# Kernel tuning notes

Hardware: AMD Instinct MI355X
Metric: run time of the kernel (lower is better)

The kernel has to match this reference:

```python
import jax, jax.numpy as jnp
import numpy as np

EMBED = 1024
HEADS = 16
HEAD_DIM = EMBED // HEADS


def setup_inputs() -> dict:
    key = jax.random.key(0)
    ks = jax.random.split(key, 12)
    N, S, E = 4, 2048, EMBED
    scale = 1.0 / np.sqrt(E)
    inp = {
        "values": jax.random.normal(ks[0], (N, S, E), dtype=jnp.float32),
        "keys": jax.random.normal(ks[1], (N, S, E), dtype=jnp.float32),
        "query": jax.random.normal(ks[2], (N, S, E), dtype=jnp.float32),
        "mask": jnp.ones((N, 1, 1, S), dtype=jnp.int32),
        # Linear params: y = x @ W + b (W stored as [in, out])
        "Wv": jax.random.normal(ks[3], (E, E), dtype=jnp.float32) * scale,
        "bv": jnp.zeros((E,), dtype=jnp.float32),
        "Wk": jax.random.normal(ks[4], (E, E), dtype=jnp.float32) * scale,
        "bk": jnp.zeros((E,), dtype=jnp.float32),
        "Wq": jax.random.normal(ks[5], (E, E), dtype=jnp.float32) * scale,
        "bq": jnp.zeros((E,), dtype=jnp.float32),
        "Wo": jax.random.normal(ks[6], (E, E), dtype=jnp.float32) * scale,
        "bo": jnp.zeros((E,), dtype=jnp.float32),
    }
    return inp


def reference(values, keys, query, mask, Wv, bv, Wk, bk, Wq, bq, Wo, bo):
    N, Q, E = query.shape
    V = values.shape[1]
    K = keys.shape[1]
    v = (values @ Wv + bv).reshape(N, V, HEADS, HEAD_DIM)
    k = (keys @ Wk + bk).reshape(N, K, HEADS, HEAD_DIM)
    q = (query @ Wq + bq).reshape(N, Q, HEADS, HEAD_DIM)
    # energy: [N, H, Q, K]
    energy = jnp.einsum("nqhd,nkhd->nhqk", q, k)
    energy = jnp.where(mask == 0, jnp.float32(-1e20), energy)
    # NOTE: original scales by sqrt(embed_size), not sqrt(head_dim)
    attn = jax.nn.softmax(energy / jnp.sqrt(jnp.float32(E)), axis=3)
    out = jnp.einsum("nhql,nlhd->nqhd", attn, v).reshape(N, Q, E)
    return out @ Wo + bo
```

## Files before the change

kernel.cpp:

```cpp
#include <hip/hip_runtime.h>

#define H 16
#define DH 64
#define S 2048
#define E 1024
#define NB 4

typedef short short8_t __attribute__((ext_vector_type(8)));
typedef float float4_t __attribute__((ext_vector_type(4)));
typedef float float16_t __attribute__((ext_vector_type(16)));

__device__ inline unsigned short f2bf(float f) {
    union { float f; unsigned u; } v; v.f = f;
    unsigned r = v.u + 0x7fffu + ((v.u >> 16) & 1u);
    return (unsigned short)(r >> 16);
}

__device__ __forceinline__ unsigned pk_bf16(float a, float b) {
    union { float f; unsigned u; } ua, ub;
    ua.f = a; ub.f = b;
    unsigned ra = ua.u + 0x7fffu + ((ua.u >> 16) & 1u);
    unsigned rb = ub.u + 0x7fffu + ((ub.u >> 16) & 1u);
    return __builtin_amdgcn_perm(rb, ra, 0x07060302u);
}

__device__ __forceinline__ unsigned cvt_pk_bf16(float a, float b) {
    unsigned r;
    asm("v_cvt_pk_bf16_f32 %0, %1, %2" : "=v"(r) : "v"(a), "v"(b));
    return r;
}

__device__ __forceinline__ float16_t mfma32(short8_t a, short8_t b, float16_t c) {
    return __builtin_amdgcn_mfma_f32_32x32x16_bf16(a, b, c, 0, 0, 0);
}

__device__ __forceinline__ void async_copy16(const unsigned short* g, unsigned short* l) {
    __builtin_amdgcn_global_load_lds(
        (const __attribute__((address_space(1))) unsigned int*)g,
        (__attribute__((address_space(3))) unsigned int*)l, 16, 0, 0);
}

__global__ __launch_bounds__(256) void xcvt_kernel(
    const float* __restrict__ v, const float* __restrict__ k,
    const float* __restrict__ q, unsigned short* __restrict__ xv,
    unsigned short* __restrict__ xk, unsigned short* __restrict__ xq)
{
    const int z = blockIdx.y;
    const float* src = (z == 0) ? v : (z == 1) ? k : q;
    unsigned short* dst = (z == 0) ? xv : (z == 1) ? xk : xq;
    size_t i0 = ((size_t)blockIdx.x * 256 + threadIdx.x) * 8;
    float4 f0 = *reinterpret_cast<const float4*>(src + i0);
    float4 f1 = *reinterpret_cast<const float4*>(src + i0 + 4);
    uint4 o;
    o.x = pk_bf16(f0.x, f0.y); o.y = pk_bf16(f0.z, f0.w);
    o.z = pk_bf16(f1.x, f1.y); o.w = pk_bf16(f1.z, f1.w);
    *reinterpret_cast<uint4*>(dst + i0) = o;
}

__global__ __launch_bounds__(256) void wcvt_kernel(
    const float* __restrict__ Wv, const float* __restrict__ Wk,
    const float* __restrict__ Wq, const float* __restrict__ Wo,
    unsigned short* __restrict__ Wt)
{
    __shared__ float tile[64][65];
    const float* W = (blockIdx.z == 0) ? Wv : (blockIdx.z == 1) ? Wk
                   : (blockIdx.z == 2) ? Wq : Wo;
    unsigned short* out = Wt + (size_t)blockIdx.z * (E * E);
    const int k0 = blockIdx.x * 64, n0 = blockIdx.y * 64;
    const int tid = threadIdx.x;
#pragma unroll
    for (int i = 0; i < 4; ++i) {
        int c = i * 256 + tid;
        int kl = c >> 4, nl4 = (c & 15) * 4;
        float4 v = *reinterpret_cast<const float4*>(W + (size_t)(k0 + kl) * E + n0 + nl4);
        tile[kl][nl4 + 0] = v.x; tile[kl][nl4 + 1] = v.y;
        tile[kl][nl4 + 2] = v.z; tile[kl][nl4 + 3] = v.w;
    }
    __syncthreads();
#pragma unroll
    for (int i = 0; i < 4; ++i) {
        int c = i * 256 + tid;
        int nl = c >> 4, kl4 = (c & 15) * 4;
        ushort4 o;
        o.x = f2bf(tile[kl4 + 0][nl]); o.y = f2bf(tile[kl4 + 1][nl]);
        o.z = f2bf(tile[kl4 + 2][nl]); o.w = f2bf(tile[kl4 + 3][nl]);
        *reinterpret_cast<ushort4*>(out + (size_t)(n0 + nl) * E + k0 + kl4) = o;
    }
}

template<int MODE>
__global__ __launch_bounds__(256) void proj_kernel(
    const unsigned short* __restrict__ A, const unsigned short* __restrict__ WT,
    const float* __restrict__ bias, unsigned short* __restrict__ out)
{
    __shared__ __align__(16) unsigned short As[2][128][64];
    __shared__ __align__(16) unsigned short Bs[2][128][64];

    const int tid = threadIdx.x;
    const int wlin = blockIdx.y * 8 + blockIdx.x;
    const int wid = (wlin & 7) * 64 + (wlin >> 3);
    const int n0 = (wid & 7) * 128;
    const int m0 = (wid >> 3) * 128;
    const int wave = tid >> 6, lane = tid & 63;
    const int wm = wave >> 1, wn = wave & 1;
    const int quad = lane >> 4, l16 = lane & 15;
    const int r8 = lane >> 3;
    const int c8 = (lane & 7) ^ (r8 & 7);

    float4_t acc[4][4];
#pragma unroll
    for (int i = 0; i < 4; ++i)
#pragma unroll
        for (int j = 0; j < 4; ++j) { float4_t z = {0.f,0.f,0.f,0.f}; acc[i][j] = z; }

#pragma unroll
    for (int j = 0; j < 4; ++j) {
        int row = wave * 32 + j * 8 + r8;
        async_copy16(A  + (size_t)(m0 + row) * E + c8 * 8, &As[0][wave * 32 + j * 8][0]);
        async_copy16(WT + (size_t)(n0 + row) * E + c8 * 8, &Bs[0][wave * 32 + j * 8][0]);
    }

    for (int it = 0; it < 16; ++it) {
        const int cur = it & 1, nxt = cur ^ 1;
        __syncthreads();

        if (it < 15) {
            const int kn = (it + 1) * 64;
#pragma unroll
            for (int j = 0; j < 4; ++j) {
                int row = wave * 32 + j * 8 + r8;
                async_copy16(A  + (size_t)(m0 + row) * E + kn + c8 * 8, &As[nxt][wave * 32 + j * 8][0]);
                async_copy16(WT + (size_t)(n0 + row) * E + kn + c8 * 8, &Bs[nxt][wave * 32 + j * 8][0]);
            }
        }
#pragma unroll
        for (int kk = 0; kk < 2; ++kk) {
            short8_t a[4], b[4];
#pragma unroll
            for (int mi = 0; mi < 4; ++mi)
                a[mi] = *reinterpret_cast<const short8_t*>(
                    &As[cur][wm * 64 + mi * 16 + l16][((kk * 4 + quad) ^ (l16 & 7)) * 8]);
#pragma unroll
            for (int nj = 0; nj < 4; ++nj)
                b[nj] = *reinterpret_cast<const short8_t*>(
                    &Bs[cur][wn * 64 + nj * 16 + l16][((kk * 4 + quad) ^ (l16 & 7)) * 8]);
#pragma unroll
            for (int x = 0; x < 4; ++x)
#pragma unroll
                for (int y = 0; y < 4; ++y) {
                    if constexpr (MODE == 0)
                        acc[x][y] = __builtin_amdgcn_mfma_f32_16x16x32_bf16(b[x], a[y], acc[x][y], 0, 0, 0);
                    else
                        acc[x][y] = __builtin_amdgcn_mfma_f32_16x16x32_bf16(a[x], b[y], acc[x][y], 0, 0, 0);
                }
        }
    }

    if constexpr (MODE == 0) {
#pragma unroll
        for (int x = 0; x < 4; ++x) {
            float4 bb = *reinterpret_cast<const float4*>(&bias[n0 + wn * 64 + x * 16 + quad * 4]);
#pragma unroll
            for (int y = 0; y < 4; ++y) {
                int m = m0 + wm * 64 + y * 16 + l16;
                int nn = m >> 11, s = m & 2047;
                int sp = (s & ~12) | (((s >> 2) & 1) << 3) | (((s >> 3) & 1) << 2);
#pragma unroll
                for (int r = 0; r < 4; ++r) {
                    int gcol = n0 + wn * 64 + x * 16 + quad * 4 + r;
                    int h = gcol >> 6, d = gcol & 63;
                    float val = acc[x][y][r] + ((const float*)&bb)[r];
                    out[(((size_t)(nn * H + h)) * DH + d) * S + sp] = f2bf(val);
                }
            }
        }
    } else {
#pragma unroll
        for (int x = 0; x < 4; ++x) {
#pragma unroll
            for (int y = 0; y < 4; ++y) {
                int gcol = n0 + wn * 64 + y * 16 + l16;
                float bvv = bias[gcol];
                int h = gcol >> 6, d = gcol & 63;
#pragma unroll
                for (int r = 0; r < 4; ++r) {
                    int gm = m0 + wm * 64 + x * 16 + quad * 4 + r;
                    float val = acc[x][y][r] + bvv;
                    int nn = gm >> 11, s = gm & 2047;
                    out[(((size_t)(nn * H + h)) * S + s) * DH + d] = f2bf(val);
                }
            }
        }
    }
}

__global__ __launch_bounds__(256, 4) void flash_kernel(
    const unsigned short* __restrict__ Qb, const unsigned short* __restrict__ Kb,
    const unsigned short* __restrict__ VTb, const int* __restrict__ mask,
    unsigned short* __restrict__ AO)
{
    __shared__ __align__(16) unsigned short Ks[2][64][64];
    __shared__ __align__(16) unsigned short Vs[2][64][64];
    __shared__ __align__(16) float am[2][64];
    __shared__ __align__(16) float lbuf[4][32];

    const int tid = threadIdx.x;
    const int wave = tid >> 6, lane = tid & 63;
    const int l32 = lane & 31, hf = lane >> 5;
    const int r8 = lane >> 3;
    const int c8 = (lane & 7) ^ (r8 & 7);

    const int wlin = blockIdx.y * 16 + blockIdx.x;
    const int wid = (wlin & 7) * 128 + (wlin >> 3);
    const int qt = wid & 15;
    const int nh = wid >> 4;
    const int n = nh >> 4, h = nh & 15;
    const size_t hb = (size_t)nh * S * DH;
    const unsigned short* Qh = Qb + hb;
    const unsigned short* Kh = Kb + hb;
    const unsigned short* Vh = VTb + hb;
    const int* mp = mask + n * S;

    const float c1 = 0.03125f * 1.4426950408889634f;
    const float C2_UNMASK = -23.083120654223414f;
    const float C2_MASK   = -1.44e20f;

    short8_t qa[4];
#pragma unroll
    for (int ks = 0; ks < 4; ++ks) {
        int row = qt * 128 + wave * 32 + l32;
        qa[ks] = *reinterpret_cast<const short8_t*>(Qh + (size_t)row * DH + ks * 16 + hf * 8);
    }

    float16_t o[2];
#pragma unroll
    for (int nb = 0; nb < 2; ++nb)
#pragma unroll
        for (int i = 0; i < 16; ++i) o[nb][i] = 0.f;
    float lsum = 0.f;

#pragma unroll
    for (int j = 0; j < 2; ++j) {
        int row = wave * 16 + j * 8 + r8;
        async_copy16(Kh + (size_t)row * DH + c8 * 8, &Ks[0][wave * 16 + j * 8][0]);
        async_copy16(Vh + (size_t)row * S + c8 * 8,  &Vs[0][wave * 16 + j * 8][0]);
    }
    if (tid < 64) am[0][tid] = (mp[tid] == 0) ? C2_MASK : C2_UNMASK;

    for (int it = 0; it < 32; ++it) {
        const int cur = it & 1, nxt = cur ^ 1;
        __syncthreads();

        const int kn = (it < 31) ? (it + 1) * 64 : 0;
#pragma unroll
        for (int j = 0; j < 2; ++j) {
            int row = wave * 16 + j * 8 + r8;
            async_copy16(Kh + (size_t)(kn + row) * DH + c8 * 8, &Ks[nxt][wave * 16 + j * 8][0]);
            async_copy16(Vh + (size_t)row * S + kn + c8 * 8,    &Vs[nxt][wave * 16 + j * 8][0]);
        }
        if (tid < 64) am[nxt][tid] = (mp[kn + tid] == 0) ? C2_MASK : C2_UNMASK;

        unsigned w[2][4][2];
#pragma unroll
        for (int kvb = 0; kvb < 2; ++kvb) {
            float16_t st;
#pragma unroll
            for (int i = 0; i < 16; ++i) st[i] = 0.f;
            __builtin_amdgcn_s_setprio(1);
#pragma unroll
            for (int ks = 0; ks < 4; ++ks) {
                short8_t ak = *reinterpret_cast<const short8_t*>(
                    &Ks[cur][kvb * 32 + l32][((ks * 2 + hf) ^ (l32 & 7)) * 8]);
                st = mfma32(ak, qa[ks], st);
            }
            __builtin_amdgcn_s_setprio(0);
#pragma unroll
            for (int g = 0; g < 4; ++g) {
                float4 c2v = *reinterpret_cast<const float4*>(&am[cur][kvb * 32 + g * 8 + hf * 4]);
                float p0 = __builtin_amdgcn_exp2f(st[g * 4 + 0] * c1 + c2v.x);
                float p1 = __builtin_amdgcn_exp2f(st[g * 4 + 1] * c1 + c2v.y);
                float p2 = __builtin_amdgcn_exp2f(st[g * 4 + 2] * c1 + c2v.z);
                float p3 = __builtin_amdgcn_exp2f(st[g * 4 + 3] * c1 + c2v.w);
                lsum += (p0 + p1) + (p2 + p3);
                w[kvb][g][0] = cvt_pk_bf16(p0, p1);
                w[kvb][g][1] = cvt_pk_bf16(p2, p3);
            }
        }

        __builtin_amdgcn_s_setprio(1);
#pragma unroll
        for (int ks2 = 0; ks2 < 4; ++ks2) {
            const int kvb = ks2 >> 1, t = ks2 & 1;
            union { unsigned u[4]; short8_t s; } pu;
            pu.u[0] = w[kvb][t * 2][0];     pu.u[1] = w[kvb][t * 2][1];
            pu.u[2] = w[kvb][t * 2 + 1][0]; pu.u[3] = w[kvb][t * 2 + 1][1];
#pragma unroll
            for (int nb = 0; nb < 2; ++nb) {
                const int d = nb * 32 + l32;
                short8_t vb = *reinterpret_cast<const short8_t*>(
                    &Vs[cur][d][((kvb * 4 + t * 2 + hf) ^ (d & 7)) * 8]);
                o[nb] = mfma32(pu.s, vb, o[nb]);
            }
        }
        __builtin_amdgcn_s_setprio(0);
    }

    lsum += __shfl_xor(lsum, 32);
    if (lane < 32) lbuf[wave][lane] = lsum;

#pragma unroll
    for (int g = 0; g < 4; ++g) {
        float4 dn = *reinterpret_cast<const float4*>(&lbuf[wave][g * 8 + hf * 4]);
#pragma unroll
        for (int r = 0; r < 4; ++r) {
            float invl = __builtin_amdgcn_rcpf(((const float*)&dn)[r]);
            int row = g * 8 + hf * 4 + r;
            int qrow = qt * 128 + wave * 32 + row;
            size_t gm = (size_t)n * S + qrow;
#pragma unroll
            for (int nb = 0; nb < 2; ++nb) {
                int col = h * DH + nb * 32 + l32;
                AO[gm * E + col] = f2bf(o[nb][g * 4 + r] * invl);
            }
        }
    }
}

__global__ __launch_bounds__(256) void ogemm_kernel(
    const unsigned short* __restrict__ A, const unsigned short* __restrict__ WT,
    const float* __restrict__ bias, float* __restrict__ out)
{
    __shared__ __align__(16) unsigned short As[2][128][64];
    __shared__ __align__(16) unsigned short Bs[2][128][64];

    const int tid = threadIdx.x;
    const int wlin = blockIdx.y * 8 + blockIdx.x;
    const int wid = (wlin & 7) * 64 + (wlin >> 3);
    const int n0 = (wid & 7) * 128;
    const int m0 = (wid >> 3) * 128;
    const int wave = tid >> 6, lane = tid & 63;
    const int wm = wave >> 1, wn = wave & 1;
    const int quad = lane >> 4, l16 = lane & 15;
    const int r8 = lane >> 3;
    const int c8 = (lane & 7) ^ (r8 & 7);

    float4_t acc[4][4];
#pragma unroll
    for (int i = 0; i < 4; ++i)
#pragma unroll
        for (int j = 0; j < 4; ++j) { float4_t z = {0.f,0.f,0.f,0.f}; acc[i][j] = z; }

#pragma unroll
    for (int j = 0; j < 4; ++j) {
        int row = wave * 32 + j * 8 + r8;
        async_copy16(A  + (size_t)(m0 + row) * E + c8 * 8, &As[0][wave * 32 + j * 8][0]);
        async_copy16(WT + (size_t)(n0 + row) * E + c8 * 8, &Bs[0][wave * 32 + j * 8][0]);
    }

    for (int it = 0; it < 16; ++it) {
        const int cur = it & 1, nxt = cur ^ 1;
        __syncthreads();

        if (it < 15) {
            const int kn = (it + 1) * 64;
#pragma unroll
            for (int j = 0; j < 4; ++j) {
                int row = wave * 32 + j * 8 + r8;
                async_copy16(A  + (size_t)(m0 + row) * E + kn + c8 * 8, &As[nxt][wave * 32 + j * 8][0]);
                async_copy16(WT + (size_t)(n0 + row) * E + kn + c8 * 8, &Bs[nxt][wave * 32 + j * 8][0]);
            }
        }
#pragma unroll
        for (int kk = 0; kk < 2; ++kk) {
            short8_t a[4], b[4];
#pragma unroll
            for (int mi = 0; mi < 4; ++mi)
                a[mi] = *reinterpret_cast<const short8_t*>(
                    &As[cur][wm * 64 + mi * 16 + l16][((kk * 4 + quad) ^ (l16 & 7)) * 8]);
#pragma unroll
            for (int nj = 0; nj < 4; ++nj)
                b[nj] = *reinterpret_cast<const short8_t*>(
                    &Bs[cur][wn * 64 + nj * 16 + l16][((kk * 4 + quad) ^ (l16 & 7)) * 8]);
#pragma unroll
            for (int mi = 0; mi < 4; ++mi)
#pragma unroll
                for (int nj = 0; nj < 4; ++nj)
                    acc[mi][nj] = __builtin_amdgcn_mfma_f32_16x16x32_bf16(a[mi], b[nj], acc[mi][nj], 0, 0, 0);
        }
    }
#pragma unroll
    for (int mi = 0; mi < 4; ++mi)
#pragma unroll
        for (int nj = 0; nj < 4; ++nj) {
            int gcol = n0 + wn * 64 + nj * 16 + l16;
            float bvv = bias[gcol];
#pragma unroll
            for (int r = 0; r < 4; ++r) {
                int gm = m0 + wm * 64 + mi * 16 + quad * 4 + r;
                out[(size_t)gm * E + gcol] = acc[mi][nj][r] + bvv;
            }
        }
}

extern "C" void kernel_launch(void* const* d_in, const int* in_sizes, int n_in,
                              void* d_out, int out_size, void* d_ws, size_t ws_size,
                              hipStream_t stream) {
    const float* values = (const float*)d_in[0];
    const float* keys   = (const float*)d_in[1];
    const float* query  = (const float*)d_in[2];
    const int*   mask   = (const int*)d_in[3];
    const float* Wv = (const float*)d_in[4];  const float* bv = (const float*)d_in[5];
    const float* Wk = (const float*)d_in[6];  const float* bk = (const float*)d_in[7];
    const float* Wq = (const float*)d_in[8];  const float* bq = (const float*)d_in[9];
    const float* Wo = (const float*)d_in[10]; const float* bo = (const float*)d_in[11];
    float* out = (float*)d_out;

    char* ws = (char*)d_ws;
    unsigned short* Wt = (unsigned short*)ws;
    unsigned short* xv = (unsigned short*)(ws + 8388608);
    unsigned short* xk = (unsigned short*)(ws + 25165824);
    unsigned short* xq = (unsigned short*)(ws + 41943040);
    unsigned short* vt = (unsigned short*)(ws + 58720256);
    unsigned short* kb = xv;
    unsigned short* qb = xk;
    unsigned short* ao = xq;

    xcvt_kernel<<<dim3(4096, 3), 256, 0, stream>>>(values, keys, query, xv, xk, xq);
    wcvt_kernel<<<dim3(16, 16, 4), 256, 0, stream>>>(Wv, Wk, Wq, Wo, Wt);
    proj_kernel<0><<<dim3(8, 64), 256, 0, stream>>>(xv, Wt,           bv, vt);
    proj_kernel<1><<<dim3(8, 64), 256, 0, stream>>>(xk, Wt + 1048576, bk, kb);
    proj_kernel<1><<<dim3(8, 64), 256, 0, stream>>>(xq, Wt + 2097152, bq, qb);
    flash_kernel<<<dim3(16, 64), 256, 0, stream>>>(qb, kb, vt, mask, ao);
    ogemm_kernel<<<dim3(8, 64), 256, 0, stream>>>(ao, Wt + 3145728, bo, out);
}
```

Before: 343.5 us.

## Fuse fp32-to-bf16 input conversion into a single batched QKV projection kernel

Drops the separate activation conversion kernel. The projection GEMM now loads fp32 inputs straight into registers, converts them to bf16 and writes them to LDS, with the next tile's loads issued before the MFMA work. The three Q/K/V projection launches become one launch using blockIdx.z, and the workgroup swizzle is removed from both the projection and output GEMMs. This saves a full round trip of the bf16 activations through HBM plus two launches, at the cost of doubled global read bytes per A tile, more register pressure, and a runtime branch on z inside the MFMA loop.

```diff
diff --git a/kernel.cpp b/kernel.cpp
--- a/kernel.cpp
+++ b/kernel.cpp
@@ -38,23 +38,6 @@
     __builtin_amdgcn_global_load_lds(
         (const __attribute__((address_space(1))) unsigned int*)g,
         (__attribute__((address_space(3))) unsigned int*)l, 16, 0, 0);
-}
-
-__global__ __launch_bounds__(256) void xcvt_kernel(
-    const float* __restrict__ v, const float* __restrict__ k,
-    const float* __restrict__ q, unsigned short* __restrict__ xv,
-    unsigned short* __restrict__ xk, unsigned short* __restrict__ xq)
-{
-    const int z = blockIdx.y;
-    const float* src = (z == 0) ? v : (z == 1) ? k : q;
-    unsigned short* dst = (z == 0) ? xv : (z == 1) ? xk : xq;
-    size_t i0 = ((size_t)blockIdx.x * 256 + threadIdx.x) * 8;
-    float4 f0 = *reinterpret_cast<const float4*>(src + i0);
-    float4 f1 = *reinterpret_cast<const float4*>(src + i0 + 4);
-    uint4 o;
-    o.x = pk_bf16(f0.x, f0.y); o.y = pk_bf16(f0.z, f0.w);
-    o.z = pk_bf16(f1.x, f1.y); o.w = pk_bf16(f1.z, f1.w);
-    *reinterpret_cast<uint4*>(dst + i0) = o;
 }
 
 __global__ __launch_bounds__(256) void wcvt_kernel(
@@ -88,35 +71,59 @@
     }
 }
 
-template<int MODE>
-__global__ __launch_bounds__(256) void proj_kernel(
-    const unsigned short* __restrict__ A, const unsigned short* __restrict__ WT,
-    const float* __restrict__ bias, unsigned short* __restrict__ out)
+__global__ __launch_bounds__(256) void qkvproj_kernel(
+    const float* __restrict__ Va, const float* __restrict__ Ka,
+    const float* __restrict__ Qa, const unsigned short* __restrict__ Wt,
+    const float* __restrict__ bv, const float* __restrict__ bk,
+    const float* __restrict__ bq, unsigned short* __restrict__ vt,
+    unsigned short* __restrict__ kbo, unsigned short* __restrict__ qbo)
 {
     __shared__ __align__(16) unsigned short As[2][128][64];
     __shared__ __align__(16) unsigned short Bs[2][128][64];
 
+    const int z = blockIdx.z;
+    const float* Ag = (z == 0) ? Va : (z == 1) ? Ka : Qa;
+    const unsigned short* WT = Wt + (size_t)z * (E * E);
+    const float* bias = (z == 0) ? bv : (z == 1) ? bk : bq;
+    unsigned short* out = (z == 0) ? vt : (z == 1) ? kbo : qbo;
+
     const int tid = threadIdx.x;
-    const int wlin = blockIdx.y * 8 + blockIdx.x;
-    const int wid = (wlin & 7) * 64 + (wlin >> 3);
-    const int n0 = (wid & 7) * 128;
-    const int m0 = (wid >> 3) * 128;
+    const int m0 = blockIdx.y * 128;
+    const int n0 = blockIdx.x * 128;
     const int wave = tid >> 6, lane = tid & 63;
     const int wm = wave >> 1, wn = wave & 1;
     const int quad = lane >> 4, l16 = lane & 15;
     const int r8 = lane >> 3;
     const int c8 = (lane & 7) ^ (r8 & 7);
+    const int ar = tid >> 3;
+    const int ac = tid & 7;
+    const int asw = (ac ^ (ar & 7)) * 8;
 
     float4_t acc[4][4];
 #pragma unroll
     for (int i = 0; i < 4; ++i)
 #pragma unroll
-        for (int j = 0; j < 4; ++j) { float4_t z = {0.f,0.f,0.f,0.f}; acc[i][j] = z; }
-
+        for (int j = 0; j < 4; ++j) { float4_t zz = {0.f,0.f,0.f,0.f}; acc[i][j] = zz; }
+
+    float4 af[4][2];
+#pragma unroll
+    for (int j = 0; j < 4; ++j) {
+        const float* src = Ag + (size_t)(m0 + j * 32 + ar) * E + ac * 8;
+        af[j][0] = *reinterpret_cast<const float4*>(src);
+        af[j][1] = *reinterpret_cast<const float4*>(src + 4);
+    }
+#pragma unroll
+    for (int j = 0; j < 4; ++j) {
+        uint4 w;
+        w.x = cvt_pk_bf16(af[j][0].x, af[j][0].y);
+        w.y = cvt_pk_bf16(af[j][0].z, af[j][0].w);
+        w.z = cvt_pk_bf16(af[j][1].x, af[j][1].y);
+        w.w = cvt_pk_bf16(af[j][1].z, af[j][1].w);
+        *reinterpret_cast<uint4*>(&As[0][j * 32 + ar][asw]) = w;
+    }
 #pragma unroll
     for (int j = 0; j < 4; ++j) {
         int row = wave * 32 + j * 8 + r8;
-        async_copy16(A  + (size_t)(m0 + row) * E + c8 * 8, &As[0][wave * 32 + j * 8][0]);
         async_copy16(WT + (size_t)(n0 + row) * E + c8 * 8, &Bs[0][wave * 32 + j * 8][0]);
     }
 
@@ -128,8 +135,13 @@
             const int kn = (it + 1) * 64;
 #pragma unroll
             for (int j = 0; j < 4; ++j) {
+                const float* src = Ag + (size_t)(m0 + j * 32 + ar) * E + kn + ac * 8;
+                af[j][0] = *reinterpret_cast<const float4*>(src);
+                af[j][1] = *reinterpret_cast<const float4*>(src + 4);
+            }
+#pragma unroll
+            for (int j = 0; j < 4; ++j) {
                 int row = wave * 32 + j * 8 + r8;
-                async_copy16(A  + (size_t)(m0 + row) * E + kn + c8 * 8, &As[nxt][wave * 32 + j * 8][0]);
                 async_copy16(WT + (size_t)(n0 + row) * E + kn + c8 * 8, &Bs[nxt][wave * 32 + j * 8][0]);
             }
         }
@@ -144,19 +156,34 @@
             for (int nj = 0; nj < 4; ++nj)
                 b[nj] = *reinterpret_cast<const short8_t*>(
                     &Bs[cur][wn * 64 + nj * 16 + l16][((kk * 4 + quad) ^ (l16 & 7)) * 8]);
-#pragma unroll
-            for (int x = 0; x < 4; ++x)
-#pragma unroll
-                for (int y = 0; y < 4; ++y) {
-                    if constexpr (MODE == 0)
+            if (z == 0) {
+#pragma unroll
+                for (int x = 0; x < 4; ++x)
+#pragma unroll
+                    for (int y = 0; y < 4; ++y)
                         acc[x][y] = __builtin_amdgcn_mfma_f32_16x16x32_bf16(b[x], a[y], acc[x][y], 0, 0, 0);
-                    else
+            } else {
+#pragma unroll
+                for (int x = 0; x < 4; ++x)
+#pragma unroll
+                    for (int y = 0; y < 4; ++y)
                         acc[x][y] = __builtin_amdgcn_mfma_f32_16x16x32_bf16(a[x], b[y], acc[x][y], 0, 0, 0);
-                }
-        }
-    }
-
-    if constexpr (MODE == 0) {
+            }
+        }
+        if (it < 15) {
+#pragma unroll
+            for (int j = 0; j < 4; ++j) {
+                uint4 w;
+                w.x = cvt_pk_bf16(af[j][0].x, af[j][0].y);
+                w.y = cvt_pk_bf16(af[j][0].z, af[j][0].w);
+                w.z = cvt_pk_bf16(af[j][1].x, af[j][1].y);
+                w.w = cvt_pk_bf16(af[j][1].z, af[j][1].w);
+                *reinterpret_cast<uint4*>(&As[nxt][j * 32 + ar][asw]) = w;
+            }
+        }
+    }
+
+    if (z == 0) {
 #pragma unroll
         for (int x = 0; x < 4; ++x) {
             float4 bb = *reinterpret_cast<const float4*>(&bias[n0 + wn * 64 + x * 16 + quad * 4]);
@@ -334,10 +361,8 @@
     __shared__ __align__(16) unsigned short Bs[2][128][64];
 
     const int tid = threadIdx.x;
-    const int wlin = blockIdx.y * 8 + blockIdx.x;
-    const int wid = (wlin & 7) * 64 + (wlin >> 3);
-    const int n0 = (wid & 7) * 128;
-    const int m0 = (wid >> 3) * 128;
+    const int m0 = blockIdx.y * 128;
+    const int n0 = blockIdx.x * 128;
     const int wave = tid >> 6, lane = tid & 63;
     const int wm = wave >> 1, wn = wave & 1;
     const int quad = lane >> 4, l16 = lane & 15;
@@ -417,19 +442,14 @@
 
     char* ws = (char*)d_ws;
     unsigned short* Wt = (unsigned short*)ws;
-    unsigned short* xv = (unsigned short*)(ws + 8388608);
-    unsigned short* xk = (unsigned short*)(ws + 25165824);
-    unsigned short* xq = (unsigned short*)(ws + 41943040);
-    unsigned short* vt = (unsigned short*)(ws + 58720256);
-    unsigned short* kb = xv;
-    unsigned short* qb = xk;
-    unsigned short* ao = xq;
-
-    xcvt_kernel<<<dim3(4096, 3), 256, 0, stream>>>(values, keys, query, xv, xk, xq);
+    unsigned short* vt = (unsigned short*)(ws + 8388608);
+    unsigned short* kb = (unsigned short*)(ws + 25165824);
+    unsigned short* qb = (unsigned short*)(ws + 41943040);
+    unsigned short* ao = (unsigned short*)(ws + 58720256);
+
     wcvt_kernel<<<dim3(16, 16, 4), 256, 0, stream>>>(Wv, Wk, Wq, Wo, Wt);
-    proj_kernel<0><<<dim3(8, 64), 256, 0, stream>>>(xv, Wt,           bv, vt);
-    proj_kernel<1><<<dim3(8, 64), 256, 0, stream>>>(xk, Wt + 1048576, bk, kb);
-    proj_kernel<1><<<dim3(8, 64), 256, 0, stream>>>(xq, Wt + 2097152, bq, qb);
+    qkvproj_kernel<<<dim3(8, 64, 3), 256, 0, stream>>>(values, keys, query, Wt,
+                                                       bv, bk, bq, vt, kb, qb);
     flash_kernel<<<dim3(16, 64), 256, 0, stream>>>(qb, kb, vt, mask, ao);
     ogemm_kernel<<<dim3(8, 64), 256, 0, stream>>>(ao, Wt + 3145728, bo, out);
 }
```

Result: slower. 363.7 us (+5.9%).
